# Performance work log

Measured on AMD Instinct MI355X. Metric: run time of the kernel, lower is better.

## Reference

```python
import jax, jax.numpy as jnp
import numpy as np

N = 4096            # number of proposals
C = 6               # classes incl. background
SCORE_TH = 0.05
NMS_TH = 0.3
DET_LIM = 100
IM_MAX = 1023.0     # clip to [0, im_size-1]
BBOX_W = jnp.array([10.0, 10.0, 10.0, 5.0, 5.0, 5.0], dtype=jnp.float32)


def setup_inputs() -> dict:
    key = jax.random.key(0)
    k1, k2, k3, k4 = jax.random.split(key, 4)
    # realistic 3D proposals inside the 1024^3 volume: lo in [0,900), size in [1,101)
    lo = jax.random.uniform(k1, (N, 3), dtype=jnp.float32) * 900.0
    sz = jax.random.uniform(k2, (N, 3), dtype=jnp.float32) * 100.0 + 1.0
    bbox_proposals = jnp.concatenate([jnp.zeros((N, 1), jnp.float32), lo, lo + sz], axis=1)  # [N,7]
    bbox_pred = jax.random.normal(k3, (N, C * 6), dtype=jnp.float32) * 0.1                   # [N,36]
    cls_score = jax.random.normal(k4, (N, C), dtype=jnp.float32)                              # [N,6]
    return {"bbox_proposals": bbox_proposals, "bbox_pred": bbox_pred, "cls_score": cls_score}


def _bbox_transform_clip(boxes, deltas):
    # boxes: [N,6] (x1,y1,z1,x2,y2,z2); deltas: [N, C*6] -> pred_boxes [N,C,6]
    d = deltas.reshape(N, C, 6) / BBOX_W
    sizes = boxes[:, 3:6] - boxes[:, 0:3] + 1.0          # [N,3]
    ctrs = boxes[:, 0:3] + 0.5 * sizes                   # [N,3]
    pred_ctr = d[:, :, :3] * sizes[:, None, :] + ctrs[:, None, :]
    pred_sz = jnp.exp(d[:, :, 3:]) * sizes[:, None, :]
    lo = jnp.clip(pred_ctr - 0.5 * pred_sz, 0.0, IM_MAX)
    hi = jnp.clip(pred_ctr + 0.5 * pred_sz - 1.0, 0.0, IM_MAX)
    return jnp.concatenate([lo, hi], axis=-1)            # [N,C,6]


def _nms_one_class(bj, sj):
    # bj: [N,6], sj: [N] -> scores with suppressed/below-threshold entries zeroed
    valid = sj > SCORE_TH
    order = jnp.argsort(-sj)
    b = bj[order]
    v = valid[order]
    l, h = b[:, :3], b[:, 3:]
    vol = jnp.prod(h - l + 1.0, axis=1)                                  # [N]
    inter = jnp.prod(
        jnp.clip(jnp.minimum(h[:, None, :], h[None, :, :])
                 - jnp.maximum(l[:, None, :], l[None, :, :]) + 1.0, 0.0, None),
        axis=-1)                                                          # [N,N]
    iou = inter / (vol[:, None] + vol[None, :] - inter)
    idx = jnp.arange(N)

    def body(i, keep):
        supp = keep[i] & (iou[i] > NMS_TH) & (idx > i)
        return keep & ~supp

    keep = jax.lax.fori_loop(0, N, body, v)
    keep_orig = jnp.zeros(N, bool).at[order].set(keep)
    return jnp.where(keep_orig, sj, 0.0)


def reference(bbox_proposals, bbox_pred, cls_score):
    scores = jax.nn.softmax(cls_score, axis=1)            # [N,C]
    boxes = bbox_proposals[:, 1:]                          # [N,6]
    pred_boxes = _bbox_transform_clip(boxes, bbox_pred)    # [N,C,6]
    cls_boxes = jnp.transpose(pred_boxes[:, 1:, :], (1, 0, 2))  # [5,N,6] (skip background)
    cls_scores = scores[:, 1:].T                                 # [5,N]
    kept = jax.vmap(_nms_one_class)(cls_boxes, cls_scores)       # [5,N]
    # top-100 detections-per-image limit (fixed-shape: zero out below image_thresh)
    thresh = jax.lax.top_k(kept.reshape(-1), DET_LIM)[0][-1]
    final = jnp.where(kept >= thresh, kept, 0.0)
    # pack boxes + final score: [5, N, 7]
    return jnp.concatenate([cls_boxes, final[:, :, None]], axis=-1)
```

## Files before the change

### kernel.cpp

```cpp
#include <hip/hip_runtime.h>
#include <stdint.h>

#define NN 4096
#define NCLS 5
#define NWORD 64
#define SCORE_TH 0.05f
#define NMS_TH 0.3f

__device__ __forceinline__ uint32_t fmap(float f) {
    uint32_t u = __float_as_uint(f);
    return (u & 0x80000000u) ? ~u : (u | 0x80000000u);
}
__device__ __forceinline__ float funmap(uint32_t m) {
    uint32_t u = (m & 0x80000000u) ? (m & 0x7fffffffu) : ~m;
    return __uint_as_float(u);
}

__device__ __forceinline__ uint64_t shfl64(uint64_t x, int src) {
    uint32_t lo = (uint32_t)x, hi = (uint32_t)(x >> 32);
    lo = __shfl(lo, src, 64);
    hi = __shfl(hi, src, 64);
    return ((uint64_t)hi << 32) | lo;
}

__global__ void k_prep(const float* __restrict__ prop, const float* __restrict__ pred,
                       const float* __restrict__ cls, float* __restrict__ out,
                       uint64_t* __restrict__ skey) {
    int i = blockIdx.x * 256 + threadIdx.x;
    if (i >= NN) return;
    const float* pr = prop + i * 7;
    float l0 = pr[1], l1 = pr[2], l2 = pr[3];
    float h0 = pr[4], h1 = pr[5], h2 = pr[6];
    float s0 = h0 - l0 + 1.f, s1 = h1 - l1 + 1.f, s2 = h2 - l2 + 1.f;
    float c0 = l0 + 0.5f * s0, c1 = l1 + 0.5f * s1, c2 = l2 + 0.5f * s2;

    float sc[6];
    float mx = -3.4e38f;
#pragma unroll
    for (int c = 0; c < 6; ++c) { sc[c] = cls[i * 6 + c]; mx = fmaxf(mx, sc[c]); }
    float sum = 0.f;
#pragma unroll
    for (int c = 0; c < 6; ++c) { sc[c] = expf(sc[c] - mx); sum += sc[c]; }
    float inv = 1.f / sum;

#pragma unroll
    for (int c = 1; c < 6; ++c) {
        const float* d = pred + i * 36 + c * 6;
        float dc0 = d[0] / 10.f, dc1 = d[1] / 10.f, dc2 = d[2] / 10.f;
        float ds0 = d[3] / 5.f, ds1 = d[4] / 5.f, ds2 = d[5] / 5.f;
        float pc0 = dc0 * s0 + c0, pc1 = dc1 * s1 + c1, pc2 = dc2 * s2 + c2;
        float ps0 = expf(ds0) * s0, ps1 = expf(ds1) * s1, ps2 = expf(ds2) * s2;
        float o0 = fminf(fmaxf(pc0 - 0.5f * ps0, 0.f), 1023.f);
        float o1 = fminf(fmaxf(pc1 - 0.5f * ps1, 0.f), 1023.f);
        float o2 = fminf(fmaxf(pc2 - 0.5f * ps2, 0.f), 1023.f);
        float o3 = fminf(fmaxf(pc0 + 0.5f * ps0 - 1.f, 0.f), 1023.f);
        float o4 = fminf(fmaxf(pc1 + 0.5f * ps1 - 1.f, 0.f), 1023.f);
        float o5 = fminf(fmaxf(pc2 + 0.5f * ps2 - 1.f, 0.f), 1023.f);
        float* ob = out + ((size_t)(c - 1) * NN + i) * 7;
        ob[0] = o0; ob[1] = o1; ob[2] = o2; ob[3] = o3; ob[4] = o4; ob[5] = o5;
        float score = sc[c] * inv;
        skey[(c - 1) * NN + i] = ((uint64_t)fmap(score) << 12) | (uint32_t)(4095 - i);
    }
}

__global__ void __launch_bounds__(256) k_sort(const uint64_t* __restrict__ skey,
                                              const float* __restrict__ out,
                                              float* __restrict__ sscores,
                                              unsigned short* __restrict__ order,
                                              float* __restrict__ sboxes) {
    int c = blockIdx.y;
    int i = blockIdx.x * 256 + threadIdx.x;
    const uint64_t* K = skey + c * NN;
    uint64_t ki = K[i];
    int r0 = 0, r1 = 0, r2 = 0, r3 = 0;
#pragma unroll 4
    for (int j = 0; j < NN; j += 4) {
        r0 += (K[j] > ki);
        r1 += (K[j + 1] > ki);
        r2 += (K[j + 2] > ki);
        r3 += (K[j + 3] > ki);
    }
    int rank = (r0 + r1) + (r2 + r3);
    int io = c * NN + rank;
    order[io] = (unsigned short)i;
    sscores[io] = funmap((uint32_t)(ki >> 12));
    const float* b = out + ((size_t)c * NN + i) * 7;
    float* sb = sboxes + (size_t)io * 6;
#pragma unroll
    for (int k = 0; k < 6; ++k) sb[k] = b[k];
}

__global__ void __launch_bounds__(256) k_mask(const float* __restrict__ sboxes,
                                              uint64_t* __restrict__ mask,
                                              uint64_t* __restrict__ diag) {
    int tid = threadIdx.x;
    int wid = tid >> 6, lane = tid & 63;
    int rb = blockIdx.y, c = blockIdx.z;
    int cb = rb + blockIdx.x * 4 + wid;
    bool active = (cb < 64);

    __shared__ float cB[4][64][6];
    __shared__ float cV[4][64];

    int r = rb * 64 + lane;
    const float* rp = sboxes + ((size_t)c * NN + r) * 6;
    float rl0 = rp[0], rl1 = rp[1], rl2 = rp[2];
    float rh0 = rp[3], rh1 = rp[4], rh2 = rp[5];
    float vi = (rh0 - rl0 + 1.f) * (rh1 - rl1 + 1.f) * (rh2 - rl2 + 1.f);

    if (active) {
        const float* cp = sboxes + ((size_t)c * NN + cb * 64 + lane) * 6;
#pragma unroll
        for (int k = 0; k < 6; ++k) cB[wid][lane][k] = cp[k];
        cV[wid][lane] = (cB[wid][lane][3] - cB[wid][lane][0] + 1.f) *
                        (cB[wid][lane][4] - cB[wid][lane][1] + 1.f) *
                        (cB[wid][lane][5] - cB[wid][lane][2] + 1.f);
    }
    __syncthreads();
    if (!active) return;

    uint64_t bits = 0;
    for (int j2 = 0; j2 < 64; ++j2) {
        int j = cb * 64 + j2;
        if (j > r) {
            float w0 = fmaxf(fminf(rh0, cB[wid][j2][3]) - fmaxf(rl0, cB[wid][j2][0]) + 1.f, 0.f);
            float w1 = fmaxf(fminf(rh1, cB[wid][j2][4]) - fmaxf(rl1, cB[wid][j2][1]) + 1.f, 0.f);
            float w2 = fmaxf(fminf(rh2, cB[wid][j2][5]) - fmaxf(rl2, cB[wid][j2][2]) + 1.f, 0.f);
            float inter = w0 * w1 * w2;
            float iou = inter / (vi + cV[wid][j2] - inter);
            if (iou > NMS_TH) bits |= 1ull << j2;
        }
    }
    mask[((size_t)c * NN + r) * NWORD + cb] = bits;
    if (cb == rb) diag[(size_t)c * NN + r] = bits;
}

__global__ void __launch_bounds__(64, 1) k_nms(const float* __restrict__ sscores,
                                               const unsigned short* __restrict__ order,
                                               const uint64_t* __restrict__ mask,
                                               const uint64_t* __restrict__ diag,
                                               float* __restrict__ kept) {
    int c = blockIdx.x;
    int lane = threadIdx.x;
    const uint64_t* M = mask + (size_t)c * NN * NWORD;
    const uint64_t* D = diag + (size_t)c * NN;
    const float* ss = sscores + c * NN;

    uint64_t remv = 0;
    {
        const float4* sl = (const float4*)(ss + lane * 64);
#pragma unroll
        for (int q = 0; q < 16; ++q) {
            float4 v = sl[q];
            if (!(v.x > SCORE_TH)) remv |= 1ull << (q * 4);
            if (!(v.y > SCORE_TH)) remv |= 1ull << (q * 4 + 1);
            if (!(v.z > SCORE_TH)) remv |= 1ull << (q * 4 + 2);
            if (!(v.w > SCORE_TH)) remv |= 1ull << (q * 4 + 3);
        }
    }

    uint64_t bufA[64], bufB[64];

#pragma unroll
    for (int b = 0; b < 64; ++b) bufA[b] = M[((size_t)b << 6) + lane];
    __builtin_amdgcn_sched_barrier(0);

    auto prefetch = [&](uint64_t* buf, int w) {
        if (w < 64) {
            const uint64_t* Mb = M + ((size_t)w << 12);
            if (lane >= w) {
#pragma unroll
                for (int b = 0; b < 64; ++b) buf[b] = Mb[((size_t)b << 6) + lane];
            }
        }
        __builtin_amdgcn_sched_barrier(0);
    };

    auto process = [&](const uint64_t* buf, int w) {
        uint64_t rws = shfl64(remv, w);
        uint32_t rlo = __builtin_amdgcn_readfirstlane((uint32_t)rws);
        uint32_t rhi = __builtin_amdgcn_readfirstlane((uint32_t)(rws >> 32));
        uint64_t rw = ((uint64_t)rhi << 32) | rlo;
        const uint64_t* Db = D + (w << 6);
        uint64_t kmask = 0;
#pragma unroll
        for (int b = 0; b < 64; ++b) {
            uint64_t dg = Db[b];
            bool keep = ((rw >> b) & 1) == 0;
            kmask |= keep ? (1ull << b) : 0ull;
            rw |= keep ? dg : 0ull;
        }
        if (lane >= w) {
#pragma unroll
            for (int b = 0; b < 64; ++b) {
                uint64_t km = ((kmask >> b) & 1) ? ~0ull : 0ull;
                remv |= buf[b] & km;
            }
        }
        __builtin_amdgcn_sched_barrier(0);
    };

#pragma unroll 1
    for (int w = 0; w < 64; w += 2) {
        prefetch(bufB, w + 1);
        process(bufA, w);
        prefetch(bufA, w + 2);
        process(bufB, w + 1);
    }

    __shared__ uint64_t sh[64];
    sh[lane] = remv;
    __syncthreads();
    const unsigned short* ord = order + c * NN;
    for (int t = 0; t < 64; ++t) {
        int p = t * 64 + lane;
        bool kp = !((sh[t] >> lane) & 1);
        float s = ss[p];
        int oi = ord[p];
        kept[c * NN + oi] = kp ? s : 0.f;
    }
}

__global__ void __launch_bounds__(1024) k_topk_final(const float* __restrict__ kept,
                                                     float* __restrict__ out) {
    int tid = threadIdx.x;
    uint32_t v[20];
#pragma unroll
    for (int k = 0; k < 20; ++k) v[k] = fmap(kept[k * 1024 + tid]);
    __shared__ int red[16];
    __shared__ int tot;
    uint32_t pre = 0;
    for (int bit = 31; bit >= 0; --bit) {
        uint32_t cand = pre | (1u << bit);
        int cnt = 0;
#pragma unroll
        for (int k = 0; k < 20; ++k) cnt += (v[k] >= cand);
#pragma unroll
        for (int off = 32; off; off >>= 1) cnt += __shfl_down(cnt, off, 64);
        if ((tid & 63) == 0) red[tid >> 6] = cnt;
        __syncthreads();
        if (tid == 0) {
            int s = 0;
            for (int q = 0; q < 16; ++q) s += red[q];
            tot = s;
        }
        __syncthreads();
        if (tot >= 100) pre = cand;
    }
#pragma unroll
    for (int k = 0; k < 20; ++k) {
        int idx = k * 1024 + tid;
        int c = idx >> 12;
        int i = idx & (NN - 1);
        out[((size_t)c * NN + i) * 7 + 6] = (v[k] >= pre) ? funmap(v[k]) : 0.f;
    }
}

extern "C" void kernel_launch(void* const* d_in, const int* in_sizes, int n_in,
                              void* d_out, int out_size, void* d_ws, size_t ws_size,
                              hipStream_t stream) {
    const float* prop = (const float*)d_in[0];
    const float* pred = (const float*)d_in[1];
    const float* cls = (const float*)d_in[2];
    float* out = (float*)d_out;

    char* base = (char*)d_ws;
    uint64_t* skey = (uint64_t*)base;
    uint64_t* diag = (uint64_t*)(base + (160ull << 10));
    float* sscores = (float*)(base + (320ull << 10));
    float* kept = (float*)(base + (400ull << 10));
    unsigned short* order = (unsigned short*)(base + (480ull << 10));
    float* sboxes = (float*)(base + (528ull << 10));
    uint64_t* mask = (uint64_t*)(base + (1ull << 20));

    k_prep<<<dim3(16), dim3(256), 0, stream>>>(prop, pred, cls, out, skey);
    k_sort<<<dim3(16, NCLS), dim3(256), 0, stream>>>(skey, out, sscores, order, sboxes);
    k_mask<<<dim3(16, 64, NCLS), dim3(256), 0, stream>>>(sboxes, mask, diag);
    k_nms<<<dim3(NCLS), dim3(64), 0, stream>>>(sscores, order, mask, diag, kept);
    k_topk_final<<<dim3(1), dim3(1024), 0, stream>>>(kept, out);
}
```

Measured before the change: 469.8 us.

## Stage NMS mask tiles and diagonal in LDS via async global-to-LDS loads

```diff
diff --git a/kernel.cpp b/kernel.cpp
--- a/kernel.cpp
+++ b/kernel.cpp
@@ -21,6 +21,12 @@
     lo = __shfl(lo, src, 64);
     hi = __shfl(hi, src, 64);
     return ((uint64_t)hi << 32) | lo;
+}
+
+__device__ __forceinline__ void gload_lds16(const void* g, void* l) {
+    __builtin_amdgcn_global_load_lds(
+        (const __attribute__((address_space(1))) uint32_t*)g,
+        (__attribute__((address_space(3))) uint32_t*)l, 16, 0, 0);
 }
 
 __global__ void k_prep(const float* __restrict__ prop, const float* __restrict__ pred,
@@ -72,15 +78,15 @@
     int i = blockIdx.x * 256 + threadIdx.x;
     const uint64_t* K = skey + c * NN;
     uint64_t ki = K[i];
-    int r0 = 0, r1 = 0, r2 = 0, r3 = 0;
-#pragma unroll 4
-    for (int j = 0; j < NN; j += 4) {
-        r0 += (K[j] > ki);
-        r1 += (K[j + 1] > ki);
-        r2 += (K[j + 2] > ki);
-        r3 += (K[j + 3] > ki);
-    }
-    int rank = (r0 + r1) + (r2 + r3);
+    int rank = 0;
+#pragma unroll 2
+    for (int j = 0; j < NN; j += 8) {
+        uint64_t k0 = K[j], k1 = K[j + 1], k2 = K[j + 2], k3 = K[j + 3];
+        uint64_t k4 = K[j + 4], k5 = K[j + 5], k6 = K[j + 6], k7 = K[j + 7];
+        int a = (k0 > ki) + (k1 > ki) + (k2 > ki) + (k3 > ki);
+        int b = (k4 > ki) + (k5 > ki) + (k6 > ki) + (k7 > ki);
+        rank += a + b;
+    }
     int io = c * NN + rank;
     order[io] = (unsigned short)i;
     sscores[io] = funmap((uint32_t)(ki >> 12));
@@ -103,12 +109,12 @@
     __shared__ float cV[4][64];
 
     int r = rb * 64 + lane;
-    const float* rp = sboxes + ((size_t)c * NN + r) * 6;
-    float rl0 = rp[0], rl1 = rp[1], rl2 = rp[2];
-    float rh0 = rp[3], rh1 = rp[4], rh2 = rp[5];
-    float vi = (rh0 - rl0 + 1.f) * (rh1 - rl1 + 1.f) * (rh2 - rl2 + 1.f);
-
+    float rl0 = 0, rl1 = 0, rl2 = 0, rh0 = 0, rh1 = 0, rh2 = 0, vi = 0;
     if (active) {
+        const float* rp = sboxes + ((size_t)c * NN + r) * 6;
+        rl0 = rp[0]; rl1 = rp[1]; rl2 = rp[2];
+        rh0 = rp[3]; rh1 = rp[4]; rh2 = rp[5];
+        vi = (rh0 - rl0 + 1.f) * (rh1 - rl1 + 1.f) * (rh2 - rl2 + 1.f);
         const float* cp = sboxes + ((size_t)c * NN + cb * 64 + lane) * 6;
 #pragma unroll
         for (int k = 0; k < 6; ++k) cB[wid][lane][k] = cp[k];
@@ -140,11 +146,28 @@
                                                const uint64_t* __restrict__ mask,
                                                const uint64_t* __restrict__ diag,
                                                float* __restrict__ kept) {
+    __shared__ __align__(16) uint64_t ltile[2][64 * 64];
+    __shared__ __align__(16) uint64_t ldiag[NN];
+    __shared__ uint64_t sh[64];
+
     int c = blockIdx.x;
     int lane = threadIdx.x;
     const uint64_t* M = mask + (size_t)c * NN * NWORD;
     const uint64_t* D = diag + (size_t)c * NN;
     const float* ss = sscores + c * NN;
+
+    {
+        const char* g = (const char*)D + lane * 16;
+        char* l = (char*)ldiag;
+#pragma unroll
+        for (int i = 0; i < 32; ++i) gload_lds16(g + i * 1024, l + i * 1024);
+    }
+    {
+        const char* g = (const char*)M + lane * 16;
+        char* l = (char*)ltile[0];
+#pragma unroll
+        for (int i = 0; i < 32; ++i) gload_lds16(g + i * 1024, l + i * 1024);
+    }
 
     uint64_t remv = 0;
     {
@@ -159,56 +182,42 @@
         }
     }
 
-    uint64_t bufA[64], bufB[64];
-
-#pragma unroll
-    for (int b = 0; b < 64; ++b) bufA[b] = M[((size_t)b << 6) + lane];
+    asm volatile("s_waitcnt vmcnt(0)" ::: "memory");
     __builtin_amdgcn_sched_barrier(0);
 
-    auto prefetch = [&](uint64_t* buf, int w) {
-        if (w < 64) {
-            const uint64_t* Mb = M + ((size_t)w << 12);
-            if (lane >= w) {
-#pragma unroll
-                for (int b = 0; b < 64; ++b) buf[b] = Mb[((size_t)b << 6) + lane];
-            }
+    int cur = 0;
+#pragma unroll 1
+    for (int w = 0; w < 64; ++w) {
+        if (w < 63) {
+            const char* g = (const char*)(M + ((size_t)(w + 1) << 12)) + lane * 16;
+            char* l = (char*)ltile[cur ^ 1];
+#pragma unroll
+            for (int i = 0; i < 32; ++i) gload_lds16(g + i * 1024, l + i * 1024);
         }
         __builtin_amdgcn_sched_barrier(0);
-    };
-
-    auto process = [&](const uint64_t* buf, int w) {
+
         uint64_t rws = shfl64(remv, w);
         uint32_t rlo = __builtin_amdgcn_readfirstlane((uint32_t)rws);
         uint32_t rhi = __builtin_amdgcn_readfirstlane((uint32_t)(rws >> 32));
         uint64_t rw = ((uint64_t)rhi << 32) | rlo;
-        const uint64_t* Db = D + (w << 6);
-        uint64_t kmask = 0;
+        const uint64_t* Dw = ldiag + (w << 6);
+        const uint64_t* T = ltile[cur];
+        uint64_t acc = 0;
 #pragma unroll
         for (int b = 0; b < 64; ++b) {
-            uint64_t dg = Db[b];
-            bool keep = ((rw >> b) & 1) == 0;
-            kmask |= keep ? (1ull << b) : 0ull;
-            rw |= keep ? dg : 0ull;
-        }
-        if (lane >= w) {
-#pragma unroll
-            for (int b = 0; b < 64; ++b) {
-                uint64_t km = ((kmask >> b) & 1) ? ~0ull : 0ull;
-                remv |= buf[b] & km;
-            }
-        }
+            uint64_t dg = Dw[b];
+            uint64_t mrow = T[(b << 6) | lane];
+            uint64_t km = ((rw >> b) & 1) ? 0ull : ~0ull;
+            rw |= dg & km;
+            acc |= mrow & km;
+        }
+        if (lane >= w) remv |= acc;
+
+        asm volatile("s_waitcnt vmcnt(0)" ::: "memory");
         __builtin_amdgcn_sched_barrier(0);
-    };
-
-#pragma unroll 1
-    for (int w = 0; w < 64; w += 2) {
-        prefetch(bufB, w + 1);
-        process(bufA, w);
-        prefetch(bufA, w + 2);
-        process(bufB, w + 1);
-    }
-
-    __shared__ uint64_t sh[64];
+        cur ^= 1;
+    }
+
     sh[lane] = remv;
     __syncthreads();
     const unsigned short* ord = order + c * NN;
```

Measured after the change: 443.6 us. 1.06x faster.
